# Kernel optimization log

Measured on AMD Instinct MI355X. Metric: run time of the kernel, lower is better.

## Reference

```python
import jax, jax.numpy as jnp
import numpy as np

DIM = 256
NUM_HEADS = 8
HEAD_DIM = DIM // NUM_HEADS
SCALE = HEAD_DIM ** -0.5


def setup_inputs() -> dict:
    key = jax.random.key(0)
    ks = jax.random.split(key, 8)
    B, C, H, W = 2, DIM, 64, 64
    s = 0.02
    return {
        "dec_feat": jax.random.normal(ks[0], (B, C, H, W), dtype=jnp.float32),
        "enc_feat": jax.random.normal(ks[1], (B, C, H, W), dtype=jnp.float32),
        "Wq": jax.random.normal(ks[2], (C, C), dtype=jnp.float32) * s,
        "bq": jnp.zeros((C,), dtype=jnp.float32),
        "Wkv": jax.random.normal(ks[3], (2 * C, C), dtype=jnp.float32) * s,
        "bkv": jnp.zeros((2 * C,), dtype=jnp.float32),
        "Wo": jax.random.normal(ks[4], (C, C), dtype=jnp.float32) * s,
        "bo": jnp.zeros((C,), dtype=jnp.float32),
    }


def reference(dec_feat, enc_feat, Wq, bq, Wkv, bkv, Wo, bo):
    B, C, H, W = dec_feat.shape
    N = H * W
    hd = HEAD_DIM
    # 1x1 convs == per-pixel linear maps over channels
    q = jnp.einsum('bchw,dc->bdhw', dec_feat, Wq) + bq[None, :, None, None]
    kv = jnp.einsum('bchw,dc->bdhw', enc_feat, Wkv) + bkv[None, :, None, None]
    k, v = jnp.split(kv, 2, axis=1)
    # [B, C, H, W] -> [B, heads, N, head_dim]
    def to_heads(x):
        return x.reshape(B, NUM_HEADS, hd, N).transpose(0, 1, 3, 2)
    qh, kh, vh = to_heads(q), to_heads(k), to_heads(v)
    attn = jnp.einsum('bhnd,bhmd->bhnm', qh, kh) * SCALE  # [B,h,N,N]
    attn = jax.nn.softmax(attn, axis=-1)
    out = jnp.einsum('bhnm,bhmd->bhnd', attn, vh)  # [B,h,N,hd]
    out = out.transpose(0, 1, 3, 2).reshape(B, C, H, W)
    out = jnp.einsum('bchw,dc->bdhw', out, Wo) + bo[None, :, None, None]
    return out
```

## Files before the change

### kernel.cpp

```cpp
#include <hip/hip_runtime.h>
#include <hip/hip_bf16.h>

#define B_ 2
#define C_ 256
#define N_ 4096
#define NH_ 8
#define HD_ 32
#define KBLK_ 128
#define SCALE_ 0.17677669529663687f
#define LOG2E_ 1.4426950408889634f

typedef __attribute__((ext_vector_type(8))) short bf16x8;
typedef __attribute__((ext_vector_type(4))) float f32x4;

__device__ inline short f2b(float f) {
    __hip_bfloat16 h = __float2bfloat16(f);
    return __builtin_bit_cast(short, h);
}

__device__ inline unsigned pk2(float a, float b) {
    unsigned r;
    asm("v_cvt_pk_bf16_f32 %0, %1, %2" : "=v"(r) : "v"(a), "v"(b));
    return r;
}

__device__ inline void gload_lds16(const short* g, short* l) {
    __builtin_amdgcn_global_load_lds(
        (const __attribute__((address_space(1))) unsigned*)g,
        (__attribute__((address_space(3))) unsigned*)l, 16, 0, 0);
}

__global__ __launch_bounds__(256) void wcvt(
    const float* __restrict__ Wq, const float* __restrict__ Wkv,
    const float* __restrict__ Wo, short* __restrict__ Wall)
{
    const int i = (blockIdx.x * 256 + threadIdx.x) * 8;
    const float* src; int off;
    if (i < 65536)       { src = Wq;  off = i; }
    else if (i < 196608) { src = Wkv; off = i - 65536; }
    else                 { src = Wo;  off = i - 196608; }
    float4 a = ((const float4*)(src + off))[0];
    float4 c = ((const float4*)(src + off))[1];
    uint2 u0, u1;
    u0.x = pk2(a.x, a.y); u0.y = pk2(a.z, a.w);
    u1.x = pk2(c.x, c.y); u1.y = pk2(c.z, c.w);
    *(uint2*)(Wall + i)     = u0;
    *(uint2*)(Wall + i + 4) = u1;
}

__global__ __launch_bounds__(256) void proj_qkv(
    const float* __restrict__ dec, const float* __restrict__ enc,
    const short* __restrict__ Wall, const float* __restrict__ bq,
    const float* __restrict__ bkv,
    short* __restrict__ Qb, short* __restrict__ Kb, short* __restrict__ Vb)
{
    const int b = blockIdx.z, y = blockIdx.y;
    const int n0 = blockIdx.x * 64;
    const bool isQ = (y < 2);
    const float* In   = isQ ? dec : enc;
    const float* bias = isQ ? bq : bkv;
    const int row0 = isQ ? y * 128 : (y - 2) * 128;
    const int wbase = y * 128;

    const int tid = threadIdx.x;
    const int w = tid >> 6, l = tid & 63, lg = l >> 4, lr = l & 15;
    const int w2 = w >> 1, w1 = w & 1;

    __shared__ short eld[4][64][40];

    f32x4 acc[4][2] = {};
    const float* Inb = In + (size_t)b * C_ * N_;

    for (int c0 = 0; c0 < C_; c0 += 32) {
        bf16x8 af[4];
        #pragma unroll
        for (int db = 0; db < 4; db++)
            af[db] = *(const bf16x8*)&Wall[
                (size_t)(wbase + w2 * 64 + db * 16 + lr) * C_ + c0 + lg * 8];
        #pragma unroll
        for (int nb = 0; nb < 2; nb++) {
            const int n = n0 + w1 * 32 + nb * 16 + lr;
            const float* ip = Inb + (size_t)(c0 + 8 * lg) * N_ + n;
            float t0 = ip[0],          t1 = ip[(size_t)N_];
            float t2 = ip[2*(size_t)N_], t3 = ip[3*(size_t)N_];
            float t4 = ip[4*(size_t)N_], t5 = ip[5*(size_t)N_];
            float t6 = ip[6*(size_t)N_], t7 = ip[7*(size_t)N_];
            union { bf16x8 v; unsigned u[4]; } bu;
            bu.u[0] = pk2(t0, t1); bu.u[1] = pk2(t2, t3);
            bu.u[2] = pk2(t4, t5); bu.u[3] = pk2(t6, t7);
            #pragma unroll
            for (int db = 0; db < 4; db++)
                acc[db][nb] = __builtin_amdgcn_mfma_f32_16x16x32_bf16(
                    af[db], bu.v, acc[db][nb], 0, 0, 0);
        }
    }

    if (y < 4) {
        const float sA = isQ ? (SCALE_ * LOG2E_) : 1.0f;
        #pragma unroll
        for (int db = 0; db < 4; db++) {
            #pragma unroll
            for (int r = 0; r < 4; r++) {
                const int dloc = w2 * 64 + db * 16 + lg * 4 + r;
                const float bs = bias[row0 + dloc];
                #pragma unroll
                for (int nb = 0; nb < 2; nb++) {
                    const int nloc = w1 * 32 + nb * 16 + lr;
                    eld[dloc >> 5][nloc][dloc & 31]
                        = f2b((acc[db][nb][r] + bs) * sA);
                }
            }
        }
        __syncthreads();
        const int hh = tid >> 6, nl = tid & 63;
        const int hbase = isQ ? y * 4 : (y - 2) * 4;
        short* dst = (isQ ? Qb : Kb)
            + (((size_t)(b * NH_ + hbase + hh) * N_) + n0 + nl) * HD_;
        #pragma unroll
        for (int i = 0; i < 4; i++)
            ((uint4*)dst)[i] = *(const uint4*)&eld[hh][nl][i * 8];
    } else {
        #pragma unroll
        for (int db = 0; db < 4; db++) {
            #pragma unroll
            for (int r = 0; r < 4; r++) {
                const int dl = row0 + w2 * 64 + db * 16 + lg * 4 + r;
                const float bs = bias[dl];
                #pragma unroll
                for (int nb = 0; nb < 2; nb++) {
                    const int n = n0 + w1 * 32 + nb * 16 + lr;
                    Vb[((size_t)(b * C_) + (dl - 256)) * N_ + n]
                        = f2b(acc[db][nb][r] + bs);
                }
            }
        }
    }
}

__global__ __launch_bounds__(512) void attn_kernel(
    const short* __restrict__ Qb, const short* __restrict__ Kb,
    const short* __restrict__ Vb, short* __restrict__ AO)
{
    const int lin = blockIdx.x + 32 * (blockIdx.y + 8 * blockIdx.z);
    const int wg  = (lin & 7) * 64 + (lin >> 3);
    const int qblk = wg & 31, h = (wg >> 5) & 7, b = wg >> 8;

    const int tid = threadIdx.x, w = tid >> 6, l = tid & 63;
    const int lg = l >> 4, lr = l & 15;
    const int q0 = qblk * 128 + w * 16;

    const short* Qp = Qb + ((size_t)(b * NH_ + h) * N_) * HD_;
    const short* Kp = Kb + ((size_t)(b * NH_ + h) * N_) * HD_;
    const short* Vp = Vb + ((size_t)(b * NH_ + h) * HD_) * N_;

    __shared__ short Kt[2][KBLK_][HD_];
    __shared__ short Vt[2][HD_][KBLK_];

    const int ksrc  = 32 * (w & 1) + 8 * lg + 4 * (w >> 1) + ((l >> 2) & 3);
    const int kslot = (l & 3) ^ ((l >> 3) & 3);

    const int krd = (lg ^ ((lr >> 1) & 3)) * 8;

    bf16x8 qf = *(const bf16x8*)&Qp[(size_t)(q0 + lr) * HD_ + lg * 8];

    f32x4 acc0 = {}, acc1 = {};
    float lsr[4] = {0.0f, 0.0f, 0.0f, 0.0f};

    const int NT = N_ / KBLK_;

    if (w < 4) {
        #pragma unroll
        for (int p = 0; p < 2; p++)
            gload_lds16(Kp + (size_t)(p * 64 + ksrc) * HD_ + kslot * 8,
                        &Kt[0][p * 64 + w * 16][0]);
    } else {
        #pragma unroll
        for (int p = 0; p < 2; p++) {
            const int vdp = p * 16 + (w - 4) * 4 + lg;
            gload_lds16(Vp + (size_t)vdp * N_ + (lr ^ (vdp & 7)) * 8,
                        &Vt[0][vdp][0]);
        }
    }
    __syncthreads();

    int cur = 0;
    for (int it = 0; it < NT; ++it) {
        if (it + 1 < NT) {
            const int m0n = (it + 1) * KBLK_;
            if (w < 4) {
                #pragma unroll
                for (int p = 0; p < 2; p++)
                    gload_lds16(Kp + (size_t)(m0n + p * 64 + ksrc) * HD_ + kslot * 8,
                                &Kt[cur ^ 1][p * 64 + w * 16][0]);
            } else {
                #pragma unroll
                for (int p = 0; p < 2; p++) {
                    const int vdp = p * 16 + (w - 4) * 4 + lg;
                    gload_lds16(Vp + (size_t)vdp * N_ + m0n + (lr ^ (vdp & 7)) * 8,
                                &Vt[cur ^ 1][vdp][0]);
                }
            }
        }

        #pragma unroll
        for (int ks = 0; ks < 2; ks++) {
            bf16x8 kf[4];
            #pragma unroll
            for (int t = 0; t < 4; t++)
                kf[t] = *(const bf16x8*)&Kt[cur][ks * 64 + 16 * t + lr][krd];

            f32x4 z = {};
            f32x4 s[4];
            __builtin_amdgcn_s_setprio(1);
            #pragma unroll
            for (int t = 0; t < 4; t++)
                s[t] = __builtin_amdgcn_mfma_f32_16x16x32_bf16(kf[t], qf, z, 0, 0, 0);
            __builtin_amdgcn_s_setprio(0);

            bf16x8 vf[2][2];
            #pragma unroll
            for (int c = 0; c < 2; c++)
                #pragma unroll
                for (int hh = 0; hh < 2; hh++)
                    vf[c][hh] = *(const bf16x8*)&Vt[cur][16 * hh + lr]
                                    [(ks * 8 + ((4 * c + lg) ^ (lr & 7))) * 8];

            float p[4][4];
            #pragma unroll
            for (int t = 0; t < 4; t++)
                #pragma unroll
                for (int r = 0; r < 4; r++) {
                    p[t][r] = __builtin_amdgcn_exp2f(s[t][r]);
                    lsr[r] += p[t][r];
                }

            __builtin_amdgcn_s_setprio(1);
            #pragma unroll
            for (int c = 0; c < 2; c++) {
                union { bf16x8 v; unsigned u[4]; } pu;
                pu.u[0] = pk2(p[c][0], p[c][1]);
                pu.u[1] = pk2(p[c][2], p[c][3]);
                pu.u[2] = pk2(p[c + 2][0], p[c + 2][1]);
                pu.u[3] = pk2(p[c + 2][2], p[c + 2][3]);
                acc0 = __builtin_amdgcn_mfma_f32_16x16x32_bf16(vf[c][0], pu.v, acc0, 0, 0, 0);
                acc1 = __builtin_amdgcn_mfma_f32_16x16x32_bf16(vf[c][1], pu.v, acc1, 0, 0, 0);
            }
            __builtin_amdgcn_s_setprio(0);
        }

        __syncthreads();
        cur ^= 1;
    }

    float lsum = (lsr[0] + lsr[1]) + (lsr[2] + lsr[3]);
    lsum += __shfl_xor(lsum, 16);
    lsum += __shfl_xor(lsum, 32);
    const float inv = 1.0f / lsum;
    uint2 o;
    o.x = pk2(acc0[0] * inv, acc0[1] * inv);
    o.y = pk2(acc0[2] * inv, acc0[3] * inv);
    *(uint2*)&AO[((size_t)b * N_ + q0 + lr) * C_ + h * HD_ + 4 * lg] = o;
    o.x = pk2(acc1[0] * inv, acc1[1] * inv);
    o.y = pk2(acc1[2] * inv, acc1[3] * inv);
    *(uint2*)&AO[((size_t)b * N_ + q0 + lr) * C_ + h * HD_ + 16 + 4 * lg] = o;
}

__global__ __launch_bounds__(256) void proj_out(
    const short* __restrict__ AO, const short* __restrict__ Wall,
    const float* __restrict__ bias, float* __restrict__ Out)
{
    const int b = blockIdx.z;
    const int n0 = blockIdx.x * 16;
    const int tid = threadIdx.x, w = tid >> 6, l = tid & 63, lg = l >> 4, lr = l & 15;

    f32x4 acc[4] = {};

    for (int c0 = 0; c0 < C_; c0 += 32) {
        bf16x8 af[4];
        #pragma unroll
        for (int db = 0; db < 4; db++)
            af[db] = *(const bf16x8*)&Wall[
                (size_t)(768 + w * 64 + db * 16 + lr) * C_ + c0 + lg * 8];
        bf16x8 bfr = *(const bf16x8*)&AO[((size_t)b * N_ + n0 + lr) * C_ + c0 + lg * 8];
        #pragma unroll
        for (int db = 0; db < 4; db++)
            acc[db] = __builtin_amdgcn_mfma_f32_16x16x32_bf16(af[db], bfr, acc[db], 0, 0, 0);
    }

    #pragma unroll
    for (int db = 0; db < 4; db++) {
        #pragma unroll
        for (int r = 0; r < 4; r++) {
            const int d = w * 64 + db * 16 + lg * 4 + r;
            Out[((size_t)(b * C_) + d) * N_ + n0 + lr] = acc[db][r] + bias[d];
        }
    }
}

extern "C" void kernel_launch(void* const* d_in, const int* in_sizes, int n_in,
                              void* d_out, int out_size, void* d_ws, size_t ws_size,
                              hipStream_t stream) {
    const float* dec = (const float*)d_in[0];
    const float* enc = (const float*)d_in[1];
    const float* Wq  = (const float*)d_in[2];
    const float* bq  = (const float*)d_in[3];
    const float* Wkv = (const float*)d_in[4];
    const float* bkv = (const float*)d_in[5];
    const float* Wo  = (const float*)d_in[6];
    const float* bo  = (const float*)d_in[7];
    float* out = (float*)d_out;

    const size_t SEG = (size_t)B_ * N_ * C_;
    short* Qb   = (short*)d_ws;
    short* Kb   = Qb + SEG;
    short* Vb   = Kb + SEG;
    short* AOb  = Vb + SEG;
    short* Wall = AOb + SEG;

    wcvt<<<128, 256, 0, stream>>>(Wq, Wkv, Wo, Wall);
    proj_qkv<<<dim3(N_ / 64, 6, B_), 256, 0, stream>>>(dec, enc, Wall, bq, bkv,
                                                       Qb, Kb, Vb);
    attn_kernel<<<dim3(N_ / 128, NH_, B_), 512, 0, stream>>>(Qb, Kb, Vb, AOb);
    proj_out<<<dim3(N_ / 16, 1, B_), 256, 0, stream>>>(AOb, Wall, bo, out);
}
```

Baseline: 93.31 us.

## Split attention keys across wave halves, two query tiles per wave, LDS combine

Restructures the attention kernel so each wave handles 32 queries (two 16-row tiles sharing each K/V fragment load), and the two halves of the workgroup process disjoint halves of the key range, combining partial accumulators and row sums through shared memory at the end. Global-to-LDS direct loads are replaced with register-staged prefetch that is written to LDS after compute. The aim is to halve LDS fragment reads per MFMA and raise MFMA density per loop iteration. In exchange it uses more registers and extra LDS for the combine, and it relies on the unnormalized exp2 softmax (no running max), which is unchanged from before.

```diff
diff --git a/kernel.cpp b/kernel.cpp
--- a/kernel.cpp
+++ b/kernel.cpp
@@ -6,7 +6,6 @@
 #define N_ 4096
 #define NH_ 8
 #define HD_ 32
-#define KBLK_ 128
 #define SCALE_ 0.17677669529663687f
 #define LOG2E_ 1.4426950408889634f
 
@@ -22,12 +21,6 @@
     unsigned r;
     asm("v_cvt_pk_bf16_f32 %0, %1, %2" : "=v"(r) : "v"(a), "v"(b));
     return r;
-}
-
-__device__ inline void gload_lds16(const short* g, short* l) {
-    __builtin_amdgcn_global_load_lds(
-        (const __attribute__((address_space(1))) unsigned*)g,
-        (__attribute__((address_space(3))) unsigned*)l, 16, 0, 0);
 }
 
 __global__ __launch_bounds__(256) void wcvt(
@@ -147,122 +140,181 @@
 
     const int tid = threadIdx.x, w = tid >> 6, l = tid & 63;
     const int lg = l >> 4, lr = l & 15;
-    const int q0 = qblk * 128 + w * 16;
+    const int q0  = qblk * 128 + (w & 3) * 32;
+    const int khq = w >> 2;
 
     const short* Qp = Qb + ((size_t)(b * NH_ + h) * N_) * HD_;
     const short* Kp = Kb + ((size_t)(b * NH_ + h) * N_) * HD_;
     const short* Vp = Vb + ((size_t)(b * NH_ + h) * HD_) * N_;
 
-    __shared__ short Kt[2][KBLK_][HD_];
-    __shared__ short Vt[2][HD_][KBLK_];
-
-    const int ksrc  = 32 * (w & 1) + 8 * lg + 4 * (w >> 1) + ((l >> 2) & 3);
-    const int kslot = (l & 3) ^ ((l >> 3) & 3);
+    __shared__ short Kt[2][2][64][32];
+    __shared__ short Vt[2][2][32][64];
+    __shared__ float cmb[4][64][20];
+
+    const int sh = tid >> 8;
+    const int su = tid & 255;
+    const int kkey = su >> 2, kslot = su & 3;
+    const int kphys = (kslot ^ ((kkey >> 1) & 3)) * 8;
+    const int ksrc = ((kkey >> 4) & 1) * 32 + ((kkey >> 2) & 3) * 8
+                   + ((kkey >> 5) & 1) * 4 + (kkey & 3);
+    const int vd = su >> 3, vslot = su & 7;
+    const int vphys = (vslot ^ (vd & 7)) * 8;
 
     const int krd = (lg ^ ((lr >> 1) & 3)) * 8;
 
-    bf16x8 qf = *(const bf16x8*)&Qp[(size_t)(q0 + lr) * HD_ + lg * 8];
-
-    f32x4 acc0 = {}, acc1 = {};
-    float lsr[4] = {0.0f, 0.0f, 0.0f, 0.0f};
-
-    const int NT = N_ / KBLK_;
-
-    if (w < 4) {
-        #pragma unroll
-        for (int p = 0; p < 2; p++)
-            gload_lds16(Kp + (size_t)(p * 64 + ksrc) * HD_ + kslot * 8,
-                        &Kt[0][p * 64 + w * 16][0]);
+    bf16x8 qf0 = *(const bf16x8*)&Qp[(size_t)(q0 + lr) * HD_ + lg * 8];
+    bf16x8 qf1 = *(const bf16x8*)&Qp[(size_t)(q0 + 16 + lr) * HD_ + lg * 8];
+
+    f32x4 accA0 = {}, accA1 = {}, accB0 = {}, accB1 = {};
+    float lsrA[4] = {0, 0, 0, 0}, lsrB[4] = {0, 0, 0, 0};
+
+    const int NT = 2048 / 64;
+
+    if (sh == 0) {
+        uint4 p0 = *(const uint4*)(Kp + (size_t)ksrc * HD_ + kslot * 8);
+        uint4 p1 = *(const uint4*)(Kp + (size_t)(2048 + ksrc) * HD_ + kslot * 8);
+        *(uint4*)&Kt[0][0][kkey][kphys] = p0;
+        *(uint4*)&Kt[0][1][kkey][kphys] = p1;
     } else {
-        #pragma unroll
-        for (int p = 0; p < 2; p++) {
-            const int vdp = p * 16 + (w - 4) * 4 + lg;
-            gload_lds16(Vp + (size_t)vdp * N_ + (lr ^ (vdp & 7)) * 8,
-                        &Vt[0][vdp][0]);
-        }
+        uint4 p0 = *(const uint4*)(Vp + (size_t)vd * N_ + vslot * 8);
+        uint4 p1 = *(const uint4*)(Vp + (size_t)vd * N_ + 2048 + vslot * 8);
+        *(uint4*)&Vt[0][0][vd][vphys] = p0;
+        *(uint4*)&Vt[0][1][vd][vphys] = p1;
     }
     __syncthreads();
 
     int cur = 0;
     for (int it = 0; it < NT; ++it) {
+        uint4 pr0, pr1;
+        const int mn = (it + 1) * 64;
         if (it + 1 < NT) {
-            const int m0n = (it + 1) * KBLK_;
-            if (w < 4) {
-                #pragma unroll
-                for (int p = 0; p < 2; p++)
-                    gload_lds16(Kp + (size_t)(m0n + p * 64 + ksrc) * HD_ + kslot * 8,
-                                &Kt[cur ^ 1][p * 64 + w * 16][0]);
+            if (sh == 0) {
+                pr0 = *(const uint4*)(Kp + (size_t)(mn + ksrc) * HD_ + kslot * 8);
+                pr1 = *(const uint4*)(Kp + (size_t)(2048 + mn + ksrc) * HD_ + kslot * 8);
             } else {
-                #pragma unroll
-                for (int p = 0; p < 2; p++) {
-                    const int vdp = p * 16 + (w - 4) * 4 + lg;
-                    gload_lds16(Vp + (size_t)vdp * N_ + m0n + (lr ^ (vdp & 7)) * 8,
-                                &Vt[cur ^ 1][vdp][0]);
-                }
-            }
-        }
-
-        #pragma unroll
-        for (int ks = 0; ks < 2; ks++) {
-            bf16x8 kf[4];
-            #pragma unroll
-            for (int t = 0; t < 4; t++)
-                kf[t] = *(const bf16x8*)&Kt[cur][ks * 64 + 16 * t + lr][krd];
-
-            f32x4 z = {};
-            f32x4 s[4];
-            __builtin_amdgcn_s_setprio(1);
-            #pragma unroll
-            for (int t = 0; t < 4; t++)
-                s[t] = __builtin_amdgcn_mfma_f32_16x16x32_bf16(kf[t], qf, z, 0, 0, 0);
-            __builtin_amdgcn_s_setprio(0);
-
-            bf16x8 vf[2][2];
-            #pragma unroll
-            for (int c = 0; c < 2; c++)
-                #pragma unroll
-                for (int hh = 0; hh < 2; hh++)
-                    vf[c][hh] = *(const bf16x8*)&Vt[cur][16 * hh + lr]
-                                    [(ks * 8 + ((4 * c + lg) ^ (lr & 7))) * 8];
-
-            float p[4][4];
-            #pragma unroll
-            for (int t = 0; t < 4; t++)
-                #pragma unroll
-                for (int r = 0; r < 4; r++) {
-                    p[t][r] = __builtin_amdgcn_exp2f(s[t][r]);
-                    lsr[r] += p[t][r];
-                }
-
-            __builtin_amdgcn_s_setprio(1);
-            #pragma unroll
-            for (int c = 0; c < 2; c++) {
-                union { bf16x8 v; unsigned u[4]; } pu;
-                pu.u[0] = pk2(p[c][0], p[c][1]);
-                pu.u[1] = pk2(p[c][2], p[c][3]);
-                pu.u[2] = pk2(p[c + 2][0], p[c + 2][1]);
-                pu.u[3] = pk2(p[c + 2][2], p[c + 2][3]);
-                acc0 = __builtin_amdgcn_mfma_f32_16x16x32_bf16(vf[c][0], pu.v, acc0, 0, 0, 0);
-                acc1 = __builtin_amdgcn_mfma_f32_16x16x32_bf16(vf[c][1], pu.v, acc1, 0, 0, 0);
-            }
-            __builtin_amdgcn_s_setprio(0);
-        }
-
+                pr0 = *(const uint4*)(Vp + (size_t)vd * N_ + mn + vslot * 8);
+                pr1 = *(const uint4*)(Vp + (size_t)vd * N_ + 2048 + mn + vslot * 8);
+            }
+        }
+
+        bf16x8 kf[4];
+        #pragma unroll
+        for (int t = 0; t < 4; t++)
+            kf[t] = *(const bf16x8*)&Kt[cur][khq][16 * t + lr][krd];
+
+        f32x4 z = {};
+        f32x4 sA[4], sB[4];
+        __builtin_amdgcn_s_setprio(1);
+        #pragma unroll
+        for (int t = 0; t < 4; t++)
+            sA[t] = __builtin_amdgcn_mfma_f32_16x16x32_bf16(kf[t], qf0, z, 0, 0, 0);
+        #pragma unroll
+        for (int t = 0; t < 4; t++)
+            sB[t] = __builtin_amdgcn_mfma_f32_16x16x32_bf16(kf[t], qf1, z, 0, 0, 0);
+        __builtin_amdgcn_s_setprio(0);
+
+        bf16x8 vf[2][2];
+        #pragma unroll
+        for (int c = 0; c < 2; c++)
+            #pragma unroll
+            for (int hh = 0; hh < 2; hh++)
+                vf[c][hh] = *(const bf16x8*)&Vt[cur][khq][16 * hh + lr]
+                                [((4 * c + lg) ^ (lr & 7)) * 8];
+
+        float pA[4][4], pB[4][4];
+        #pragma unroll
+        for (int t = 0; t < 4; t++)
+            #pragma unroll
+            for (int r = 0; r < 4; r++) {
+                pA[t][r] = __builtin_amdgcn_exp2f(sA[t][r]);
+                lsrA[r] += pA[t][r];
+                pB[t][r] = __builtin_amdgcn_exp2f(sB[t][r]);
+                lsrB[r] += pB[t][r];
+            }
+
+        __builtin_amdgcn_s_setprio(1);
+        #pragma unroll
+        for (int c = 0; c < 2; c++) {
+            union { bf16x8 v; unsigned u[4]; } pu;
+            pu.u[0] = pk2(pA[c][0], pA[c][1]);
+            pu.u[1] = pk2(pA[c][2], pA[c][3]);
+            pu.u[2] = pk2(pA[c + 2][0], pA[c + 2][1]);
+            pu.u[3] = pk2(pA[c + 2][2], pA[c + 2][3]);
+            accA0 = __builtin_amdgcn_mfma_f32_16x16x32_bf16(vf[c][0], pu.v, accA0, 0, 0, 0);
+            accA1 = __builtin_amdgcn_mfma_f32_16x16x32_bf16(vf[c][1], pu.v, accA1, 0, 0, 0);
+        }
+        #pragma unroll
+        for (int c = 0; c < 2; c++) {
+            union { bf16x8 v; unsigned u[4]; } pu;
+            pu.u[0] = pk2(pB[c][0], pB[c][1]);
+            pu.u[1] = pk2(pB[c][2], pB[c][3]);
+            pu.u[2] = pk2(pB[c + 2][0], pB[c + 2][1]);
+            pu.u[3] = pk2(pB[c + 2][2], pB[c + 2][3]);
+            accB0 = __builtin_amdgcn_mfma_f32_16x16x32_bf16(vf[c][0], pu.v, accB0, 0, 0, 0);
+            accB1 = __builtin_amdgcn_mfma_f32_16x16x32_bf16(vf[c][1], pu.v, accB1, 0, 0, 0);
+        }
+        __builtin_amdgcn_s_setprio(0);
+
+        if (it + 1 < NT) {
+            if (sh == 0) {
+                *(uint4*)&Kt[cur ^ 1][0][kkey][kphys] = pr0;
+                *(uint4*)&Kt[cur ^ 1][1][kkey][kphys] = pr1;
+            } else {
+                *(uint4*)&Vt[cur ^ 1][0][vd][vphys] = pr0;
+                *(uint4*)&Vt[cur ^ 1][1][vd][vphys] = pr1;
+            }
+        }
         __syncthreads();
         cur ^= 1;
     }
 
-    float lsum = (lsr[0] + lsr[1]) + (lsr[2] + lsr[3]);
-    lsum += __shfl_xor(lsum, 16);
-    lsum += __shfl_xor(lsum, 32);
-    const float inv = 1.0f / lsum;
-    uint2 o;
-    o.x = pk2(acc0[0] * inv, acc0[1] * inv);
-    o.y = pk2(acc0[2] * inv, acc0[3] * inv);
-    *(uint2*)&AO[((size_t)b * N_ + q0 + lr) * C_ + h * HD_ + 4 * lg] = o;
-    o.x = pk2(acc1[0] * inv, acc1[1] * inv);
-    o.y = pk2(acc1[2] * inv, acc1[3] * inv);
-    *(uint2*)&AO[((size_t)b * N_ + q0 + lr) * C_ + h * HD_ + 16 + 4 * lg] = o;
+    float lsumA = (lsrA[0] + lsrA[1]) + (lsrA[2] + lsrA[3]);
+    float lsumB = (lsrB[0] + lsrB[1]) + (lsrB[2] + lsrB[3]);
+
+    if (w >= 4) {
+        float* p = &cmb[w - 4][l][0];
+        *(f32x4*)(p + 0)  = accA0;  *(f32x4*)(p + 4)  = accA1;
+        *(f32x4*)(p + 8)  = accB0;  *(f32x4*)(p + 12) = accB1;
+        p[16] = lsumA; p[17] = lsumB;
+    }
+    __syncthreads();
+    if (w < 4) {
+        const float* p = &cmb[w][l][0];
+        f32x4 o0 = *(const f32x4*)(p + 0),  o1 = *(const f32x4*)(p + 4);
+        f32x4 o2 = *(const f32x4*)(p + 8),  o3 = *(const f32x4*)(p + 12);
+        #pragma unroll
+        for (int r = 0; r < 4; r++) {
+            accA0[r] += o0[r]; accA1[r] += o1[r];
+            accB0[r] += o2[r]; accB1[r] += o3[r];
+        }
+        lsumA += p[16]; lsumB += p[17];
+
+        lsumA += __shfl_xor(lsumA, 16);
+        lsumA += __shfl_xor(lsumA, 32);
+        lsumB += __shfl_xor(lsumB, 16);
+        lsumB += __shfl_xor(lsumB, 32);
+
+        {
+            const float inv = 1.0f / lsumA;
+            uint2 o;
+            o.x = pk2(accA0[0] * inv, accA0[1] * inv);
+            o.y = pk2(accA0[2] * inv, accA0[3] * inv);
+            *(uint2*)&AO[((size_t)b * N_ + q0 + lr) * C_ + h * HD_ + 4 * lg] = o;
+            o.x = pk2(accA1[0] * inv, accA1[1] * inv);
+            o.y = pk2(accA1[2] * inv, accA1[3] * inv);
+            *(uint2*)&AO[((size_t)b * N_ + q0 + lr) * C_ + h * HD_ + 16 + 4 * lg] = o;
+        }
+        {
+            const float inv = 1.0f / lsumB;
+            uint2 o;
+            o.x = pk2(accB0[0] * inv, accB0[1] * inv);
+            o.y = pk2(accB0[2] * inv, accB0[3] * inv);
+            *(uint2*)&AO[((size_t)b * N_ + q0 + 16 + lr) * C_ + h * HD_ + 4 * lg] = o;
+            o.x = pk2(accB1[0] * inv, accB1[1] * inv);
+            o.y = pk2(accB1[2] * inv, accB1[3] * inv);
+            *(uint2*)&AO[((size_t)b * N_ + q0 + 16 + lr) * C_ + h * HD_ + 16 + 4 * lg] = o;
+        }
+    }
 }
 
 __global__ __launch_bounds__(256) void proj_out(
```

Result: faster. 89.23 us (-4.4%).
